# Performance work log

Measured on AMD Instinct MI355X. Metric: run time of the kernel, lower is better.

## Reference

```python
import jax, jax.numpy as jnp
import numpy as np

NUM_EXECUTORS = 50
NUM_DAG_FEATURES = 3
EMB_DAG = 16
EMB_GLOB = 16
HIDDEN = [64, 64, 32]
B = 60000            # number of jobs (one per env in the batched rollout)
NODES_PER_JOB = 10
NODE_FEAT = 5


def _init_mlp(key, dims):
    ws, bs = [], []
    for i in range(len(dims) - 1):
        key, k = jax.random.split(key)
        scale = 1.0 / np.sqrt(dims[i])
        ws.append(jax.random.uniform(k, (dims[i], dims[i + 1]), jnp.float32, -scale, scale))
        bs.append(jnp.zeros((dims[i + 1],), jnp.float32))
    return ws, bs


def setup_inputs() -> dict:
    rng = np.random.default_rng(0)
    n_nodes = B * NODES_PER_JOB
    # dag_batch.ptr: job i owns nodes [i*NODES_PER_JOB, (i+1)*NODES_PER_JOB)
    ptr = np.arange(B + 1, dtype=np.int64) * NODES_PER_JOB
    job_indices = rng.permutation(B).astype(np.int64)
    # ragged action counts per job (exec_mask is a prefix mask of length num_exec_acts[i])
    num_exec_acts = rng.integers(1, NUM_EXECUTORS + 1, size=B).astype(np.int64)
    n_sel = num_exec_acts[job_indices]
    T = int(n_sel.sum())
    # per-ragged-row executor index: concat([arange(n) for n in n_sel]), vectorized
    starts = np.cumsum(n_sel) - n_sel
    exec_act_idx = (np.arange(T, dtype=np.int64) - np.repeat(starts, n_sel)).astype(np.int64)

    key = jax.random.key(0)
    k_x, k_hd, k_hg, k_mlp = jax.random.split(key, 4)
    x = jax.random.normal(k_x, (n_nodes, NODE_FEAT), jnp.float32)
    h_dag = jax.random.normal(k_hd, (B, EMB_DAG), jnp.float32)
    h_glob = jax.random.normal(k_hg, (B, EMB_GLOB), jnp.float32)

    in_dim = NUM_DAG_FEATURES + EMB_DAG + EMB_GLOB + 1  # 36
    ws, bs = _init_mlp(k_mlp, [in_dim] + HIDDEN + [1])

    return {
        "x": x,
        "h_dag": h_dag,
        "h_glob": h_glob,
        "ptr": jnp.asarray(ptr),
        "job_indices": jnp.asarray(job_indices),
        "num_exec_acts": jnp.asarray(num_exec_acts),
        "exec_act_idx": jnp.asarray(exec_act_idx),
        "W1": ws[0], "b1": bs[0],
        "W2": ws[1], "b2": bs[1],
        "W3": ws[2], "b3": bs[2],
        "W4": ws[3], "b4": bs[3],
    }


def reference(x, h_dag, h_glob, ptr, job_indices, num_exec_acts, exec_act_idx,
              W1, b1, W2, b2, W3, b3, W4, b4):
    T = exec_act_idx.shape[0]                       # total ragged action rows (static)
    J = job_indices.shape[0]
    # masked gather: dag features at each dag's start node, then select jobs
    x_dag = x[ptr[:-1], :NUM_DAG_FEATURES][job_indices]        # [J, 3]
    h_dag_sel = h_dag[job_indices]                              # [J, 16]
    x_h_dag = jnp.concatenate([x_dag, h_dag_sel], axis=1)       # [J, 19]
    # variable repeat_interleave -> gather by repeated row index
    n_sel = num_exec_acts[job_indices]
    rpt = jnp.repeat(jnp.arange(J), n_sel, total_repeat_length=T)
    x_h_rpt = x_h_dag[rpt]                                      # [T, 19]
    h_glob_rpt = h_glob[rpt]                                    # [T, 16]
    # exec action feature: k / num_executors for the k-th valid executor
    exec_actions = (exec_act_idx.astype(x.dtype) / NUM_EXECUTORS)[:, None]  # [T, 1]
    h = jnp.concatenate([x_h_rpt, h_glob_rpt, exec_actions], axis=1)        # [T, 36]
    h = jax.nn.relu(h @ W1 + b1)
    h = jax.nn.relu(h @ W2 + b2)
    h = jax.nn.relu(h @ W3 + b3)
    scores = (h @ W4 + b4).squeeze(-1)                          # [T]
    return scores
```

## Files before the change

kernel.cpp:

```cpp
#include <hip/hip_runtime.h>

#define TPB 256

using half8  = __attribute__((ext_vector_type(8))) _Float16;
using fp16x2 = __attribute__((ext_vector_type(2))) __fp16;
using f32x4  = __attribute__((ext_vector_type(4))) float;

static __device__ __forceinline__ unsigned short h2u(_Float16 h) {
    union { _Float16 h; unsigned short u; } v; v.h = h; return v.u;
}
static __device__ __forceinline__ unsigned pkrtz(float a, float b) {
    fp16x2 h = __builtin_amdgcn_cvt_pkrtz(a, b);
    return __builtin_bit_cast(unsigned, h);
}
template <int CTRL>
static __device__ __forceinline__ float dppmov(float x) {
    return __int_as_float(__builtin_amdgcn_mov_dpp(__float_as_int(x), CTRL, 0xF, 0xF, true));
}
#define DPP_SWAP 0xB1

__global__ __launch_bounds__(TPB) void k_prep(const float* __restrict__ x,
                                              const float* __restrict__ h_dag,
                                              const float* __restrict__ h_glob,
                                              const int* __restrict__ ptr,
                                              const int* __restrict__ job_indices,
                                              const int* __restrict__ num_exec_acts,
                                              int J, int nb,
                                              unsigned int* __restrict__ feat,
                                              int* __restrict__ bsum, int* __restrict__ jsv,
                                              const float* __restrict__ W1,
                                              const float* __restrict__ b1,
                                              const float* __restrict__ W2,
                                              const float* __restrict__ b2,
                                              const float* __restrict__ W3,
                                              const float* __restrict__ b3,
                                              const float* __restrict__ W4,
                                              uint4* __restrict__ wfrag,
                                              float4* __restrict__ bfrag)
{
    if (blockIdx.x == (unsigned)nb) {
        if (threadIdx.x < 64) {
            int lane = threadIdx.x;
            int n = lane & 15, q = lane >> 4;
#pragma unroll
            for (int nt = 0; nt < 4; nt++) {
#pragma unroll
                for (int s = 0; s < 2; s++) {
                    half8 w1f, w2f;
#pragma unroll
                    for (int jj = 0; jj < 8; jj++) {
                        int ks = s * 32 + q * 8 + jj;
                        w1f[jj] = (ks < 36) ? (_Float16)W1[ks * 64 + nt * 16 + n] : (_Float16)0.0f;
                        w2f[jj] = (_Float16)W2[ks * 64 + nt * 16 + n];
                    }
                    wfrag[(nt * 2 + s) * 64 + lane]     = __builtin_bit_cast(uint4, w1f);
                    wfrag[(8 + nt * 2 + s) * 64 + lane] = __builtin_bit_cast(uint4, w2f);
                }
            }
#pragma unroll
            for (int nt = 0; nt < 2; nt++) {
#pragma unroll
                for (int s = 0; s < 2; s++) {
                    half8 w3f;
#pragma unroll
                    for (int jj = 0; jj < 8; jj++) {
                        int ks = s * 32 + q * 8 + jj;
                        w3f[jj] = (_Float16)W3[ks * 32 + nt * 16 + n];
                    }
                    wfrag[(16 + nt * 2 + s) * 64 + lane] = __builtin_bit_cast(uint4, w3f);
                }
            }
            bfrag[0 * 64 + lane] = make_float4(b1[n], b1[16 + n], b1[32 + n], b1[48 + n]);
            bfrag[1 * 64 + lane] = make_float4(b2[n], b2[16 + n], b2[32 + n], b2[48 + n]);
            bfrag[2 * 64 + lane] = make_float4(b3[n], b3[16 + n], W4[n], W4[16 + n]);
        }
        return;
    }

    __shared__ int sc[TPB];
    int j = blockIdx.x * TPB + threadIdx.x;
    int v = 0;
    if (j < J) {
        int ji   = job_indices[j];
        v        = num_exec_acts[ji];
        int node = ptr[ji];
        float f[40];
        f[0] = x[node * 5 + 0];
        f[1] = x[node * 5 + 1];
        f[2] = x[node * 5 + 2];
#pragma unroll
        for (int c = 0; c < 16; c++) f[3 + c]  = h_dag[ji * 16 + c];
#pragma unroll
        for (int c = 0; c < 16; c++) f[19 + c] = h_glob[j * 16 + c];
#pragma unroll
        for (int c = 35; c < 40; c++) f[c] = 0.0f;
        unsigned int w[20];
#pragma unroll
        for (int k = 0; k < 20; k++)
            w[k] = (unsigned)h2u((_Float16)f[2 * k]) | ((unsigned)h2u((_Float16)f[2 * k + 1]) << 16);
        uint4* dst = (uint4*)(feat + (size_t)j * 20);
#pragma unroll
        for (int qq = 0; qq < 5; qq++)
            dst[qq] = make_uint4(w[4 * qq], w[4 * qq + 1], w[4 * qq + 2], w[4 * qq + 3]);
    }
    sc[threadIdx.x] = v;
    __syncthreads();
    for (int d = 1; d < TPB; d <<= 1) {
        int add = (threadIdx.x >= d) ? sc[threadIdx.x - d] : 0;
        __syncthreads();
        sc[threadIdx.x] += add;
        __syncthreads();
    }
    if (j < J) jsv[j] = ((sc[threadIdx.x] - v) << 6) | v;
    if (threadIdx.x == TPB - 1) bsum[blockIdx.x] = sc[TPB - 1];
}

__global__ __launch_bounds__(TPB) void k_mlp_mfma(const unsigned int* __restrict__ feat,
                                                  const int* __restrict__ jsv,
                                                  const int* __restrict__ bsum,
                                                  const uint4* __restrict__ wfrag,
                                                  const float4* __restrict__ bfrag,
                                                  const float* __restrict__ b4,
                                                  float* __restrict__ out,
                                                  int T, int J, int nb, int numTiles, int chunk)
{
    __shared__ __align__(16) char smem[4 * 4096];
    __shared__ int boffs[TPB];
    __shared__ int swin[4][64];
    const int tid  = threadIdx.x;
    const int lane = tid & 63;
    const int wv   = tid >> 6;
    const int n    = lane & 15;
    const int q    = lane >> 4;
    char* slab = smem + wv * 4096;

    {
        int v = (tid < nb) ? bsum[tid] : 0;
        boffs[tid] = v;
        __syncthreads();
        for (int d = 1; d < TPB; d <<= 1) {
            int add = (tid >= d) ? boffs[tid - d] : 0;
            __syncthreads();
            boffs[tid] += add;
            __syncthreads();
        }
        int ex = boffs[tid] - v;
        __syncthreads();
        boffs[tid] = ex;
        __syncthreads();
    }

    half8 bw1[4][2], bw2[4][2], bw3[2][2];
#pragma unroll
    for (int nt = 0; nt < 4; nt++)
#pragma unroll
        for (int s = 0; s < 2; s++) {
            bw1[nt][s] = __builtin_bit_cast(half8, wfrag[(nt * 2 + s) * 64 + lane]);
            bw2[nt][s] = __builtin_bit_cast(half8, wfrag[(8 + nt * 2 + s) * 64 + lane]);
        }
#pragma unroll
    for (int nt = 0; nt < 2; nt++)
#pragma unroll
        for (int s = 0; s < 2; s++)
            bw3[nt][s] = __builtin_bit_cast(half8, wfrag[(16 + nt * 2 + s) * 64 + lane]);

    float4 bf1 = bfrag[0 * 64 + lane];
    float4 bf2 = bfrag[1 * 64 + lane];
    float4 bf3 = bfrag[2 * 64 + lane];
    float bb1[4] = {bf1.x, bf1.y, bf1.z, bf1.w};
    float bb2[4] = {bf2.x, bf2.y, bf2.z, bf2.w};
    float bb3[2] = {bf3.x, bf3.y};
    const float w4a = bf3.z, w4b = bf3.w;
    const float b4v = b4[0];
    const int   swr = (n >> 1) & 7;
    const int   odd = n & 1;

    const int t0 = blockIdx.x * chunk;
    const int t1 = (t0 + chunk < numTiles) ? (t0 + chunk) : numTiles;

    int j_lo;
    {
        int r0 = t0 * 128 + wv * 32;
        int lo = 0, hi = nb - 1;
        while (lo < hi) {
            int mid = (lo + hi + 1) >> 1;
            if (boffs[mid] <= r0) lo = mid; else hi = mid - 1;
        }
        j_lo = lo << 8;
    }

    for (int tile = t0; tile < t1; ++tile) {
        const int rowbase = tile * 128 + wv * 32;

        for (;;) {
            int jj = j_lo + lane;
            int s  = (jj < J) ? (boffs[jj >> 8] + (jsv[jj] >> 6)) : 0x7fffffff;
            unsigned long long m = __ballot(s <= rowbase);
            if (m == ~0ULL) { j_lo += 63; continue; }
            j_lo += 63 - __builtin_clzll(m);
            break;
        }
        {
            int jj = j_lo + lane;
            int s  = (jj < J) ? (boffs[jj >> 8] + (jsv[jj] >> 6)) : 0x7fffffff;
            swin[wv][lane] = s;
        }

        half8 a1[2][2];
#pragma unroll
        for (int mt = 0; mt < 2; mt++) {
            int  rt    = rowbase + 16 * mt + n;
            bool valid = rt < T;
            int l = 0;
#pragma unroll
            for (int stp = 32; stp; stp >>= 1) {
                int cand = l + stp;
                if (cand < 64 && swin[wv][cand] <= rt) l = cand;
            }
            int j     = j_lo + l;
            if (j > J - 1) j = J - 1;
            int start = swin[wv][l];
            const uint4* fsrc = (const uint4*)(feat + (size_t)j * 20);
            uint4 g0 = fsrc[q];
            a1[mt][0] = __builtin_bit_cast(half8, g0);
            uint4 g1 = make_uint4(0, 0, 0, 0);
            if (q == 0) {
                g1 = fsrc[4];
                float fe = valid ? (float)(rt - start) * 0.02f : 0.0f;
                g1.y = (g1.y & 0xffffu) | ((unsigned)h2u((_Float16)fe) << 16);
            }
            a1[mt][1] = __builtin_bit_cast(half8, g1);
        }

#pragma unroll
        for (int mt = 0; mt < 2; mt++) {
            f32x4 acc[4];
#pragma unroll
            for (int nt = 0; nt < 4; nt++) { f32x4 c; c[0]=c[1]=c[2]=c[3]=bb1[nt]; acc[nt]=c; }
#pragma unroll
            for (int s = 0; s < 2; s++) {
#pragma unroll
                for (int nt = 0; nt < 4; nt++)
                    acc[nt] = __builtin_amdgcn_mfma_f32_16x16x32_f16(a1[mt][s], bw1[nt][s], acc[nt], 0, 0, 0);
            }
            unsigned* sl = (unsigned*)slab;
#pragma unroll
            for (int nt = 0; nt < 4; nt++) {
                float v0 = fmaxf(acc[nt][0], 0.0f), v1 = fmaxf(acc[nt][1], 0.0f);
                float v2 = fmaxf(acc[nt][2], 0.0f), v3 = fmaxf(acc[nt][3], 0.0f);
                float t0_ = dppmov<DPP_SWAP>(v0), t1_ = dppmov<DPP_SWAP>(v1);
                float t2_ = dppmov<DPP_SWAP>(v2), t3_ = dppmov<DPP_SWAP>(v3);
                unsigned u0 = pkrtz(odd ? t2_ : v0, odd ? v2 : t0_);
                unsigned u1 = pkrtz(odd ? t3_ : v1, odd ? v3 : t1_);
                int rowA = 16 * mt + 4 * q + (odd ? 2 : 0);
                int c    = 2 * nt + (n >> 3);
                int a0   = (rowA * 8 + (c ^ ((rowA >> 1) & 7))) * 4 + ((n >> 1) & 3);
                sl[a0] = u0; sl[a0 + 32] = u1;
            }
        }

#pragma unroll
        for (int mt = 0; mt < 2; mt++) {
            const int M0 = 16 * mt;
            f32x4 acc[4];
#pragma unroll
            for (int nt = 0; nt < 4; nt++) { f32x4 c; c[0]=c[1]=c[2]=c[3]=bb2[nt]; acc[nt]=c; }
#pragma unroll
            for (int s = 0; s < 2; s++) {
                half8 a = *(const half8*)(slab + ((M0 + n) * 8 + ((s * 4 + q) ^ swr)) * 16);
#pragma unroll
                for (int nt = 0; nt < 4; nt++)
                    acc[nt] = __builtin_amdgcn_mfma_f32_16x16x32_f16(a, bw2[nt][s], acc[nt], 0, 0, 0);
            }
            unsigned* sl = (unsigned*)slab;
#pragma unroll
            for (int nt = 0; nt < 4; nt++) {
                float v0 = fmaxf(acc[nt][0], 0.0f), v1 = fmaxf(acc[nt][1], 0.0f);
                float v2 = fmaxf(acc[nt][2], 0.0f), v3 = fmaxf(acc[nt][3], 0.0f);
                float t0_ = dppmov<DPP_SWAP>(v0), t1_ = dppmov<DPP_SWAP>(v1);
                float t2_ = dppmov<DPP_SWAP>(v2), t3_ = dppmov<DPP_SWAP>(v3);
                unsigned u0 = pkrtz(odd ? t2_ : v0, odd ? v2 : t0_);
                unsigned u1 = pkrtz(odd ? t3_ : v1, odd ? v3 : t1_);
                int rowA = M0 + 4 * q + (odd ? 2 : 0);
                int c    = 2 * nt + (n >> 3);
                int a0   = (rowA * 8 + (c ^ ((rowA >> 1) & 7))) * 4 + ((n >> 1) & 3);
                sl[a0] = u0; sl[a0 + 32] = u1;
            }
        }

#pragma unroll
        for (int mt = 0; mt < 2; mt++) {
            const int M0 = 16 * mt;
            f32x4 acc[2];
#pragma unroll
            for (int nt = 0; nt < 2; nt++) { f32x4 c; c[0]=c[1]=c[2]=c[3]=bb3[nt]; acc[nt]=c; }
#pragma unroll
            for (int s = 0; s < 2; s++) {
                half8 a = *(const half8*)(slab + ((M0 + n) * 8 + ((s * 4 + q) ^ swr)) * 16);
#pragma unroll
                for (int nt = 0; nt < 2; nt++)
                    acc[nt] = __builtin_amdgcn_mfma_f32_16x16x32_f16(a, bw3[nt][s], acc[nt], 0, 0, 0);
            }
            f32x4 red;
#pragma unroll
            for (int r = 0; r < 4; r++)
                red[r] = fmaxf(acc[0][r], 0.0f) * w4a + fmaxf(acc[1][r], 0.0f) * w4b;
#pragma unroll
            for (int r = 0; r < 4; r++) {
                red[r] += dppmov<0x121>(red[r]);
                red[r] += dppmov<0x122>(red[r]);
                red[r] += dppmov<0x124>(red[r]);
                red[r] += dppmov<0x128>(red[r]);
            }
            int t = rowbase + M0 + q * 4 + n;
            float val = (n == 0) ? red[0] : (n == 1) ? red[1] : (n == 2) ? red[2] : red[3];
            if (n < 4 && t < T) out[t] = val + b4v;
        }
    }
}

extern "C" void kernel_launch(void* const* d_in, const int* in_sizes, int n_in,
                              void* d_out, int out_size, void* d_ws, size_t ws_size,
                              hipStream_t stream)
{
    const float* x             = (const float*)d_in[0];
    const float* h_dag         = (const float*)d_in[1];
    const float* h_glob        = (const float*)d_in[2];
    const int*   ptr           = (const int*)d_in[3];
    const int*   job_indices   = (const int*)d_in[4];
    const int*   num_exec_acts = (const int*)d_in[5];
    const float* W1 = (const float*)d_in[7];
    const float* b1 = (const float*)d_in[8];
    const float* W2 = (const float*)d_in[9];
    const float* b2 = (const float*)d_in[10];
    const float* W3 = (const float*)d_in[11];
    const float* b3 = (const float*)d_in[12];
    const float* W4 = (const float*)d_in[13];
    const float* b4 = (const float*)d_in[14];
    float* out = (float*)d_out;

    int J  = in_sizes[4];
    int T  = in_sizes[6];
    int nb = (J + TPB - 1) / TPB;

    char* wsp = (char*)d_ws;
    int* bsum = (int*)wsp;
    wsp += (((size_t)nb * 4) + 255) / 256 * 256;
    int* jsv = (int*)wsp;
    wsp += (((size_t)J * 4) + 255) / 256 * 256;
    uint4* wfrag = (uint4*)wsp;
    wsp += 20 * 64 * 16;
    float4* bfrag = (float4*)wsp;
    wsp += 3 * 64 * 16;
    unsigned int* feat = (unsigned int*)wsp;

    k_prep<<<nb + 1, TPB, 0, stream>>>(x, h_dag, h_glob, ptr, job_indices, num_exec_acts,
                                       J, nb, feat, bsum, jsv,
                                       W1, b1, W2, b2, W3, b3, W4, wfrag, bfrag);

    int numTiles = (T + 127) / 128;
    int grid = numTiles < 1280 ? numTiles : 1280;
    int chunk = (numTiles + grid - 1) / grid;
    grid = (numTiles + chunk - 1) / chunk;
    k_mlp_mfma<<<grid, TPB, 0, stream>>>(feat, jsv, bsum, wfrag, bfrag, b4,
                                         out, T, J, nb, numTiles, chunk);
}
```

Measured before the change: 188.7 us.

## Give each wave a contiguous row range and reuse the job-start window across tiles

The MLP kernel now hands each wave one contiguous span of rows, instead of interleaving waves across 128-row tiles. The ballot-based window of job start offsets is refreshed only when the current 32 rows pass the window's last entry. Per-row job lookup is done once per row by 32 lanes and shared through a small LDS array, rather than every lane repeating the binary search. The prep kernel also loads h_dag and h_glob as float4 vectors. The aim is to cut repeated global jsv/boffs loads, ballot loops and redundant searches, at the cost of some added LDS traffic and load-balance assumptions within each block.

Measured after the change: 181.4 us. 3.9% less time.

```diff
diff --git a/kernel.cpp b/kernel.cpp
--- a/kernel.cpp
+++ b/kernel.cpp
@@ -88,10 +88,18 @@
         f[0] = x[node * 5 + 0];
         f[1] = x[node * 5 + 1];
         f[2] = x[node * 5 + 2];
-#pragma unroll
-        for (int c = 0; c < 16; c++) f[3 + c]  = h_dag[ji * 16 + c];
-#pragma unroll
-        for (int c = 0; c < 16; c++) f[19 + c] = h_glob[j * 16 + c];
+        float4 hd[4], hg[4];
+#pragma unroll
+        for (int c4 = 0; c4 < 4; c4++) hd[c4] = *(const float4*)(h_dag + (size_t)ji * 16 + 4 * c4);
+#pragma unroll
+        for (int c4 = 0; c4 < 4; c4++) hg[c4] = *(const float4*)(h_glob + (size_t)j * 16 + 4 * c4);
+#pragma unroll
+        for (int c4 = 0; c4 < 4; c4++) {
+            f[3 + 4 * c4 + 0]  = hd[c4].x; f[3 + 4 * c4 + 1]  = hd[c4].y;
+            f[3 + 4 * c4 + 2]  = hd[c4].z; f[3 + 4 * c4 + 3]  = hd[c4].w;
+            f[19 + 4 * c4 + 0] = hg[c4].x; f[19 + 4 * c4 + 1] = hg[c4].y;
+            f[19 + 4 * c4 + 2] = hg[c4].z; f[19 + 4 * c4 + 3] = hg[c4].w;
+        }
 #pragma unroll
         for (int c = 35; c < 40; c++) f[c] = 0.0f;
         unsigned int w[20];
@@ -127,6 +135,7 @@
     __shared__ __align__(16) char smem[4 * 4096];
     __shared__ int boffs[TPB];
     __shared__ int swin[4][64];
+    __shared__ int srow[4][32];
     const int tid  = threadIdx.x;
     const int lane = tid & 63;
     const int wv   = tid >> 6;
@@ -177,144 +186,153 @@
 
     const int t0 = blockIdx.x * chunk;
     const int t1 = (t0 + chunk < numTiles) ? (t0 + chunk) : numTiles;
-
-    int j_lo;
-    {
-        int r0 = t0 * 128 + wv * 32;
-        int lo = 0, hi = nb - 1;
-        while (lo < hi) {
-            int mid = (lo + hi + 1) >> 1;
-            if (boffs[mid] <= r0) lo = mid; else hi = mid - 1;
-        }
-        j_lo = lo << 8;
-    }
-
-    for (int tile = t0; tile < t1; ++tile) {
-        const int rowbase = tile * 128 + wv * 32;
-
-        for (;;) {
-            int jj = j_lo + lane;
-            int s  = (jj < J) ? (boffs[jj >> 8] + (jsv[jj] >> 6)) : 0x7fffffff;
-            unsigned long long m = __ballot(s <= rowbase);
-            if (m == ~0ULL) { j_lo += 63; continue; }
-            j_lo += 63 - __builtin_clzll(m);
-            break;
-        }
+    const int R  = (t1 - t0) * 32;
+    const int r0 = t0 * 128 + wv * R;
+    int rend = r0 + R;
+    if (rend > T) rend = T;
+
+    if (r0 < rend) {
+        int j_lo;
         {
-            int jj = j_lo + lane;
-            int s  = (jj < J) ? (boffs[jj >> 8] + (jsv[jj] >> 6)) : 0x7fffffff;
-            swin[wv][lane] = s;
-        }
-
-        half8 a1[2][2];
-#pragma unroll
-        for (int mt = 0; mt < 2; mt++) {
-            int  rt    = rowbase + 16 * mt + n;
-            bool valid = rt < T;
-            int l = 0;
-#pragma unroll
-            for (int stp = 32; stp; stp >>= 1) {
-                int cand = l + stp;
-                if (cand < 64 && swin[wv][cand] <= rt) l = cand;
-            }
-            int j     = j_lo + l;
-            if (j > J - 1) j = J - 1;
-            int start = swin[wv][l];
-            const uint4* fsrc = (const uint4*)(feat + (size_t)j * 20);
-            uint4 g0 = fsrc[q];
-            a1[mt][0] = __builtin_bit_cast(half8, g0);
-            uint4 g1 = make_uint4(0, 0, 0, 0);
-            if (q == 0) {
-                g1 = fsrc[4];
-                float fe = valid ? (float)(rt - start) * 0.02f : 0.0f;
-                g1.y = (g1.y & 0xffffu) | ((unsigned)h2u((_Float16)fe) << 16);
-            }
-            a1[mt][1] = __builtin_bit_cast(half8, g1);
-        }
-
-#pragma unroll
-        for (int mt = 0; mt < 2; mt++) {
-            f32x4 acc[4];
-#pragma unroll
-            for (int nt = 0; nt < 4; nt++) { f32x4 c; c[0]=c[1]=c[2]=c[3]=bb1[nt]; acc[nt]=c; }
-#pragma unroll
-            for (int s = 0; s < 2; s++) {
-#pragma unroll
-                for (int nt = 0; nt < 4; nt++)
-                    acc[nt] = __builtin_amdgcn_mfma_f32_16x16x32_f16(a1[mt][s], bw1[nt][s], acc[nt], 0, 0, 0);
-            }
-            unsigned* sl = (unsigned*)slab;
-#pragma unroll
-            for (int nt = 0; nt < 4; nt++) {
-                float v0 = fmaxf(acc[nt][0], 0.0f), v1 = fmaxf(acc[nt][1], 0.0f);
-                float v2 = fmaxf(acc[nt][2], 0.0f), v3 = fmaxf(acc[nt][3], 0.0f);
-                float t0_ = dppmov<DPP_SWAP>(v0), t1_ = dppmov<DPP_SWAP>(v1);
-                float t2_ = dppmov<DPP_SWAP>(v2), t3_ = dppmov<DPP_SWAP>(v3);
-                unsigned u0 = pkrtz(odd ? t2_ : v0, odd ? v2 : t0_);
-                unsigned u1 = pkrtz(odd ? t3_ : v1, odd ? v3 : t1_);
-                int rowA = 16 * mt + 4 * q + (odd ? 2 : 0);
-                int c    = 2 * nt + (n >> 3);
-                int a0   = (rowA * 8 + (c ^ ((rowA >> 1) & 7))) * 4 + ((n >> 1) & 3);
-                sl[a0] = u0; sl[a0 + 32] = u1;
-            }
-        }
-
-#pragma unroll
-        for (int mt = 0; mt < 2; mt++) {
-            const int M0 = 16 * mt;
-            f32x4 acc[4];
-#pragma unroll
-            for (int nt = 0; nt < 4; nt++) { f32x4 c; c[0]=c[1]=c[2]=c[3]=bb2[nt]; acc[nt]=c; }
-#pragma unroll
-            for (int s = 0; s < 2; s++) {
-                half8 a = *(const half8*)(slab + ((M0 + n) * 8 + ((s * 4 + q) ^ swr)) * 16);
-#pragma unroll
-                for (int nt = 0; nt < 4; nt++)
-                    acc[nt] = __builtin_amdgcn_mfma_f32_16x16x32_f16(a, bw2[nt][s], acc[nt], 0, 0, 0);
-            }
-            unsigned* sl = (unsigned*)slab;
-#pragma unroll
-            for (int nt = 0; nt < 4; nt++) {
-                float v0 = fmaxf(acc[nt][0], 0.0f), v1 = fmaxf(acc[nt][1], 0.0f);
-                float v2 = fmaxf(acc[nt][2], 0.0f), v3 = fmaxf(acc[nt][3], 0.0f);
-                float t0_ = dppmov<DPP_SWAP>(v0), t1_ = dppmov<DPP_SWAP>(v1);
-                float t2_ = dppmov<DPP_SWAP>(v2), t3_ = dppmov<DPP_SWAP>(v3);
-                unsigned u0 = pkrtz(odd ? t2_ : v0, odd ? v2 : t0_);
-                unsigned u1 = pkrtz(odd ? t3_ : v1, odd ? v3 : t1_);
-                int rowA = M0 + 4 * q + (odd ? 2 : 0);
-                int c    = 2 * nt + (n >> 3);
-                int a0   = (rowA * 8 + (c ^ ((rowA >> 1) & 7))) * 4 + ((n >> 1) & 3);
-                sl[a0] = u0; sl[a0 + 32] = u1;
-            }
-        }
-
-#pragma unroll
-        for (int mt = 0; mt < 2; mt++) {
-            const int M0 = 16 * mt;
-            f32x4 acc[2];
-#pragma unroll
-            for (int nt = 0; nt < 2; nt++) { f32x4 c; c[0]=c[1]=c[2]=c[3]=bb3[nt]; acc[nt]=c; }
-#pragma unroll
-            for (int s = 0; s < 2; s++) {
-                half8 a = *(const half8*)(slab + ((M0 + n) * 8 + ((s * 4 + q) ^ swr)) * 16);
-#pragma unroll
-                for (int nt = 0; nt < 2; nt++)
-                    acc[nt] = __builtin_amdgcn_mfma_f32_16x16x32_f16(a, bw3[nt][s], acc[nt], 0, 0, 0);
-            }
-            f32x4 red;
-#pragma unroll
-            for (int r = 0; r < 4; r++)
-                red[r] = fmaxf(acc[0][r], 0.0f) * w4a + fmaxf(acc[1][r], 0.0f) * w4b;
-#pragma unroll
-            for (int r = 0; r < 4; r++) {
-                red[r] += dppmov<0x121>(red[r]);
-                red[r] += dppmov<0x122>(red[r]);
-                red[r] += dppmov<0x124>(red[r]);
-                red[r] += dppmov<0x128>(red[r]);
-            }
-            int t = rowbase + M0 + q * 4 + n;
-            float val = (n == 0) ? red[0] : (n == 1) ? red[1] : (n == 2) ? red[2] : red[3];
-            if (n < 4 && t < T) out[t] = val + b4v;
+            int lo = 0, hi = nb - 1;
+            while (lo < hi) {
+                int mid = (lo + hi + 1) >> 1;
+                if (boffs[mid] <= r0) lo = mid; else hi = mid - 1;
+            }
+            j_lo = lo << 8;
+        }
+        int sreg    = 0;
+        int win_top = 0x80000000;
+
+        for (int rb = r0; rb < rend; rb += 32) {
+            if (win_top <= rb + 31) {
+                for (;;) {
+                    int jj = j_lo + lane;
+                    sreg = (jj < J) ? (boffs[jj >> 8] + (jsv[jj] >> 6)) : 0x7fffffff;
+                    unsigned long long m = __ballot(sreg <= rb);
+                    int adv = 63 - __builtin_clzll(m);
+                    j_lo += adv;
+                    if (adv == 0) break;
+                }
+                swin[wv][lane] = sreg;
+                win_top = __shfl(sreg, 63);
+            }
+
+            if (lane < 32) {
+                int rt = rb + lane;
+                const int* sw = swin[wv];
+                int lj = 0;
+#pragma unroll
+                for (int stp = 32; stp; stp >>= 1) {
+                    int c = lj + stp;
+                    if (c < 64 && sw[c] <= rt) lj = c;
+                }
+                srow[wv][lane] = (lj << 8) | (rt - sw[lj]);
+            }
+
+            half8 a1[2][2];
+#pragma unroll
+            for (int mt = 0; mt < 2; mt++) {
+                int  rt    = rb + 16 * mt + n;
+                bool valid = rt < T;
+                int  u     = srow[wv][16 * mt + n];
+                int  jj2   = j_lo + (u >> 8);
+                const uint4* fsrc = (const uint4*)(feat + (size_t)jj2 * 20);
+                uint4 g0 = fsrc[q];
+                a1[mt][0] = __builtin_bit_cast(half8, g0);
+                uint4 g1 = make_uint4(0, 0, 0, 0);
+                if (q == 0) {
+                    g1 = fsrc[4];
+                    float fe = valid ? (float)(u & 255) * 0.02f : 0.0f;
+                    g1.y = (g1.y & 0xffffu) | ((unsigned)h2u((_Float16)fe) << 16);
+                }
+                a1[mt][1] = __builtin_bit_cast(half8, g1);
+            }
+
+#pragma unroll
+            for (int mt = 0; mt < 2; mt++) {
+                f32x4 acc[4];
+#pragma unroll
+                for (int nt = 0; nt < 4; nt++) { f32x4 c; c[0]=c[1]=c[2]=c[3]=bb1[nt]; acc[nt]=c; }
+#pragma unroll
+                for (int s = 0; s < 2; s++) {
+#pragma unroll
+                    for (int nt = 0; nt < 4; nt++)
+                        acc[nt] = __builtin_amdgcn_mfma_f32_16x16x32_f16(a1[mt][s], bw1[nt][s], acc[nt], 0, 0, 0);
+                }
+                unsigned* sl = (unsigned*)slab;
+#pragma unroll
+                for (int nt = 0; nt < 4; nt++) {
+                    float v0 = fmaxf(acc[nt][0], 0.0f), v1 = fmaxf(acc[nt][1], 0.0f);
+                    float v2 = fmaxf(acc[nt][2], 0.0f), v3 = fmaxf(acc[nt][3], 0.0f);
+                    float t0_ = dppmov<DPP_SWAP>(v0), t1_ = dppmov<DPP_SWAP>(v1);
+                    float t2_ = dppmov<DPP_SWAP>(v2), t3_ = dppmov<DPP_SWAP>(v3);
+                    unsigned u0 = pkrtz(odd ? t2_ : v0, odd ? v2 : t0_);
+                    unsigned u1 = pkrtz(odd ? t3_ : v1, odd ? v3 : t1_);
+                    int rowA = 16 * mt + 4 * q + (odd ? 2 : 0);
+                    int c    = 2 * nt + (n >> 3);
+                    int a0   = (rowA * 8 + (c ^ ((rowA >> 1) & 7))) * 4 + ((n >> 1) & 3);
+                    sl[a0] = u0; sl[a0 + 32] = u1;
+                }
+            }
+
+#pragma unroll
+            for (int mt = 0; mt < 2; mt++) {
+                const int M0 = 16 * mt;
+                f32x4 acc[4];
+#pragma unroll
+                for (int nt = 0; nt < 4; nt++) { f32x4 c; c[0]=c[1]=c[2]=c[3]=bb2[nt]; acc[nt]=c; }
+#pragma unroll
+                for (int s = 0; s < 2; s++) {
+                    half8 a = *(const half8*)(slab + ((M0 + n) * 8 + ((s * 4 + q) ^ swr)) * 16);
+#pragma unroll
+                    for (int nt = 0; nt < 4; nt++)
+                        acc[nt] = __builtin_amdgcn_mfma_f32_16x16x32_f16(a, bw2[nt][s], acc[nt], 0, 0, 0);
+                }
+                unsigned* sl = (unsigned*)slab;
+#pragma unroll
+                for (int nt = 0; nt < 4; nt++) {
+                    float v0 = fmaxf(acc[nt][0], 0.0f), v1 = fmaxf(acc[nt][1], 0.0f);
+                    float v2 = fmaxf(acc[nt][2], 0.0f), v3 = fmaxf(acc[nt][3], 0.0f);
+                    float t0_ = dppmov<DPP_SWAP>(v0), t1_ = dppmov<DPP_SWAP>(v1);
+                    float t2_ = dppmov<DPP_SWAP>(v2), t3_ = dppmov<DPP_SWAP>(v3);
+                    unsigned u0 = pkrtz(odd ? t2_ : v0, odd ? v2 : t0_);
+                    unsigned u1 = pkrtz(odd ? t3_ : v1, odd ? v3 : t1_);
+                    int rowA = M0 + 4 * q + (odd ? 2 : 0);
+                    int c    = 2 * nt + (n >> 3);
+                    int a0   = (rowA * 8 + (c ^ ((rowA >> 1) & 7))) * 4 + ((n >> 1) & 3);
+                    sl[a0] = u0; sl[a0 + 32] = u1;
+                }
+            }
+
+#pragma unroll
+            for (int mt = 0; mt < 2; mt++) {
+                const int M0 = 16 * mt;
+                f32x4 acc[2];
+#pragma unroll
+                for (int nt = 0; nt < 2; nt++) { f32x4 c; c[0]=c[1]=c[2]=c[3]=bb3[nt]; acc[nt]=c; }
+#pragma unroll
+                for (int s = 0; s < 2; s++) {
+                    half8 a = *(const half8*)(slab + ((M0 + n) * 8 + ((s * 4 + q) ^ swr)) * 16);
+#pragma unroll
+                    for (int nt = 0; nt < 2; nt++)
+                        acc[nt] = __builtin_amdgcn_mfma_f32_16x16x32_f16(a, bw3[nt][s], acc[nt], 0, 0, 0);
+                }
+                f32x4 red;
+#pragma unroll
+                for (int r = 0; r < 4; r++)
+                    red[r] = fmaxf(acc[0][r], 0.0f) * w4a + fmaxf(acc[1][r], 0.0f) * w4b;
+#pragma unroll
+                for (int r = 0; r < 4; r++) {
+                    red[r] += dppmov<0x121>(red[r]);
+                    red[r] += dppmov<0x122>(red[r]);
+                    red[r] += dppmov<0x124>(red[r]);
+                    red[r] += dppmov<0x128>(red[r]);
+                }
+                int t = rb + M0 + q * 4 + n;
+                float val = (n == 0) ? red[0] : (n == 1) ? red[1] : (n == 2) ? red[2] : red[3];
+                if (n < 4 && t < T) out[t] = val + b4v;
+            }
         }
     }
 }
```
